# Kernel tuning notes

Measured on AMD Instinct MI355X. Metric: run time of the kernel, lower is better.

Reference implementation:

```python
import jax, jax.numpy as jnp
import numpy as np

B, N, R = 2, 16384, 2048
CA, CS, CP, H = 128, 256, 16, 4
WQ, WK = 32, 128
NW = N // WQ
CH = CA // H
INF = 1e8


def _ln(x, w=None, b=None, eps=1e-5):
    m = jnp.mean(x, axis=-1, keepdims=True)
    v = jnp.var(x, axis=-1, keepdims=True)
    y = (x - m) * jax.lax.rsqrt(v + eps)
    if w is not None:
        y = y * w
    if b is not None:
        y = y + b
    return y


def _gather_res(x, idx):
    # x: [B, R, C], idx: [B, N] -> [B, N, C]  (torch.gather dim=1)
    return jnp.take_along_axis(x, idx[..., None], axis=1)


def _adaln(s, cond, idx, ln_w, Wg, bg, Wb):
    s = _ln(s)                      # LayerNorm, no affine
    cond = _ln(cond, ln_w)          # LayerNorm, weight only
    gate = _gather_res(cond @ Wg + bg, idx)
    bias = _gather_res(cond @ Wb, idx)
    return s * jax.nn.sigmoid(gate) + bias


def setup_inputs():
    key = jax.random.key(0)
    ks = jax.random.split(key, 20)

    def nrm(k, shape, scale=0.02):
        return jax.random.normal(k, shape, jnp.float32) * scale

    # key-window validity mask (keys are wk-wide windows centered on each wq query window)
    centers = np.arange(NW) * WQ + WQ // 2
    kidx = centers[:, None] - WK // 2 + np.arange(WK)[None, :]
    valid = (kidx >= 0) & (kidx < N)                              # [NW, WK]
    atompair_mask = jnp.broadcast_to(jnp.asarray(valid)[None, :, None, :], (B, NW, WQ, WK))

    return dict(
        atom_features=jax.random.normal(ks[0], (B, N, CA), jnp.float32),
        res_features=jax.random.normal(ks[1], (B, R, CS), jnp.float32),
        atompair_features=jax.random.normal(ks[2], (B, NW, WQ, WK, CP), jnp.float32),
        atom_res_idx=jnp.sort(jax.random.randint(ks[3], (B, N), 0, R), axis=1),
        atompos_mask=jnp.ones((B, N), jnp.float32),
        atompair_mask=atompair_mask,
        # attention AdaLN
        a_ln_w=jnp.ones((CS,), jnp.float32),
        a_Wg=nrm(ks[4], (CS, CA)), a_bg=jnp.zeros((CA,), jnp.float32), a_Wb=nrm(ks[5], (CS, CA)),
        # q / kv projections
        q_W=nrm(ks[6], (CA, CA)), q_b=jnp.zeros((CA,), jnp.float32), kv_W=nrm(ks[7], (CA, 2 * CA)),
        # pair bias head: LayerNorm(c_atompair) + Linear(c_atompair -> H, no bias)
        bij_ln_w=jnp.ones((CP,), jnp.float32), bij_ln_b=jnp.zeros((CP,), jnp.float32), bij_W=nrm(ks[8], (CP, H)),
        # residue-conditioned output gate (bias init -2)
        sg_W=nrm(ks[9], (CS, CA)), sg_b=jnp.full((CA,), -2.0, jnp.float32),
        # transition AdaLN + SwiGLU + cond gate
        t_ln_w=jnp.ones((CS,), jnp.float32),
        t_Wg=nrm(ks[10], (CS, CA)), t_bg=jnp.zeros((CA,), jnp.float32), t_Wb=nrm(ks[11], (CS, CA)),
        t_W1=nrm(ks[12], (CA, 2 * CA)), t_W2=nrm(ks[13], (CA, 2 * CA)),
        t_Wc=nrm(ks[14], (CS, CA)), t_bc=jnp.full((CA,), -2.0, jnp.float32),
        t_Wo=nrm(ks[15], (2 * CA, CA)),
    )


def reference(atom_features, res_features, atompair_features, atom_res_idx,
              atompos_mask, atompair_mask,
              a_ln_w, a_Wg, a_bg, a_Wb,
              q_W, q_b, kv_W,
              bij_ln_w, bij_ln_b, bij_W,
              sg_W, sg_b,
              t_ln_w, t_Wg, t_bg, t_Wb,
              t_W1, t_W2, t_Wc, t_bc, t_Wo):
    B_, N_ = atom_features.shape[0], atom_features.shape[1]
    # to_keys index: wk-wide key window centered on each query window (clamped; mask handles edges)
    centers = jnp.arange(NW) * WQ + WQ // 2
    kidx = jnp.clip(centers[:, None] - WK // 2 + jnp.arange(WK)[None, :], 0, N_ - 1)  # [NW, WK]

    # --- attention ---
    s = _adaln(atom_features, res_features, atom_res_idx, a_ln_w, a_Wg, a_bg, a_Wb)
    q = (s @ q_W + q_b).reshape(B_, NW, WQ, H, CH)                 # to_queries + unflatten
    kv = jnp.take(s @ kv_W, kidx, axis=1)                          # to_keys -> [B, NW, WK, 2*CA]
    kv = kv.reshape(B_, NW, WK, 2 * H, CH)
    k, v = kv[..., :H, :], kv[..., H:, :]
    a = jnp.einsum('bnqhc,bnkhc->bnqkh', q, k) / np.sqrt(CH)
    b_ij = _ln(atompair_features, bij_ln_w, bij_ln_b) @ bij_W      # [B, NW, WQ, WK, H]
    a = a + b_ij - INF * (1.0 - atompair_mask.astype(a.dtype)[..., None])
    p = jax.nn.softmax(a, axis=3)                                  # softmax over keys
    attn_out = jnp.einsum('bnqkh,bnkhc->bnqhc', p, v).reshape(B_, N_, CA)
    gate = jax.nn.sigmoid(res_features @ sg_W + sg_b)              # raw res_features (no LN)
    attn_out = attn_out * _gather_res(gate, atom_res_idx)

    atom = atom_features + attn_out * atompos_mask[..., None]

    # --- gather-conditioned transition ---
    t = _adaln(atom, res_features, atom_res_idx, t_ln_w, t_Wg, t_bg, t_Wb)
    b = jax.nn.silu(t @ t_W1) * (t @ t_W2)                          # SwiGLU, n=2
    tg = jax.nn.sigmoid(_gather_res(res_features @ t_Wc + t_bc, atom_res_idx))
    trans = tg * (b @ t_Wo)

    return atom + trans * atompos_mask[..., None]
```

## Files before the change

### kernel.cpp

```cpp
#include <hip/hip_runtime.h>
#include <hip/hip_bf16.h>
#include <string.h>

namespace {

constexpr int Bc  = 2;
constexpr int Nc  = 16384;
constexpr int Rc  = 2048;
constexpr int CAc = 128;
constexpr int CSc = 256;
constexpr int CPc = 16;
constexpr int Hc  = 4;
constexpr int WQc = 32;
constexpr int WKc = 128;
constexpr int NWc = 512;
constexpr float EPSf     = 1e-5f;
constexpr float NEG_INF  = -1e8f;
constexpr float QK_SCALE = 0.17677669529663687f;

constexpr int VT_STRIDE = 16512;
constexpr int VT_BATCH  = 128 * VT_STRIDE;

typedef short bf16x8 __attribute__((ext_vector_type(8)));
typedef float f32x4 __attribute__((ext_vector_type(4)));
typedef unsigned int u32x4 __attribute__((ext_vector_type(4)));

__device__ __forceinline__ float wsum(float v) {
#pragma unroll
  for (int m = 1; m < 64; m <<= 1) v += __shfl_xor(v, m, 64);
  return v;
}
__device__ __forceinline__ float sigm(float x) { return 1.0f / (1.0f + __expf(-x)); }
__device__ __forceinline__ float f4c(const float4& v, int i) {
  return i == 0 ? v.x : i == 1 ? v.y : i == 2 ? v.z : v.w;
}
__device__ __forceinline__ unsigned short bfx(float v) {
  __hip_bfloat16 h = __float2bfloat16(v);
  unsigned short u;
  memcpy(&u, &h, 2);
  return u;
}
__device__ __forceinline__ unsigned pk2(float a, float b) {
  return (unsigned)bfx(a) | ((unsigned)bfx(b) << 16);
}
__device__ __forceinline__ float ubf(unsigned us) {
  unsigned v = us << 16;
  float f;
  memcpy(&f, &v, 4);
  return f;
}
__device__ __forceinline__ bf16x8 ldfrag(const ushort* p) {
  return __builtin_bit_cast(bf16x8, *(const u32x4*)p);
}

__global__ void k_pack_resln(const float* __restrict__ q_W, const float* __restrict__ kv_W,
                             const float* __restrict__ t_W1, const float* __restrict__ t_W2,
                             const float* __restrict__ t_Wo,
                             ushort* __restrict__ qWt, ushort* __restrict__ kvWt,
                             ushort* __restrict__ midWt, ushort* __restrict__ WoT,
                             ushort* __restrict__ vT,
                             const float* __restrict__ res, const float* __restrict__ a_ln_w,
                             const float* __restrict__ t_ln_w, float* __restrict__ lnA,
                             float* __restrict__ lnT) {
  if (blockIdx.x < 704) {
    const int i = blockIdx.x * 256 + threadIdx.x;
    if (i < 16384) {
      const int n = i >> 7, k = i & 127;
      qWt[i] = bfx(q_W[k * 128 + n]);
    } else if (i < 49152) {
      const int i2 = i - 16384;
      const int n = i2 >> 7, k = i2 & 127;
      kvWt[i2] = bfx(kv_W[k * 256 + n]);
    } else if (i < 114688) {
      const int i3 = i - 49152;
      const int n = i3 >> 7, k = i3 & 127;
      midWt[i3] = bfx(n < 256 ? t_W1[k * 256 + n] : t_W2[k * 256 + (n - 256)]);
    } else if (i < 147456) {
      const int i4 = i - 114688;
      const int n = i4 >> 8, k = i4 & 255;
      WoT[i4] = bfx(t_Wo[k * 128 + n]);
    } else if (i < 180224) {
      const int j = i - 147456;
      const int b = j >> 14, rem = j & 16383;
      const int d = rem >> 7, p = rem & 127;
      const int col = (p < 64) ? p : (16384 + p);
      vT[(size_t)b * VT_BATCH + (size_t)d * VT_STRIDE + col] = 0;
    }
  } else {
    const int wid = threadIdx.x >> 6, lane = threadIdx.x & 63;
    const int row = (blockIdx.x - 704) * 4 + wid;
    const float* r = res + (size_t)row * CSc;
    float x[4], s = 0.f, sq = 0.f;
#pragma unroll
    for (int i = 0; i < 4; ++i) { x[i] = r[lane + 64 * i]; s += x[i]; sq += x[i] * x[i]; }
    s = wsum(s); sq = wsum(sq);
    const float mn = s * (1.0f / CSc);
    const float var = sq * (1.0f / CSc) - mn * mn;
    const float rs = rsqrtf(var + EPSf);
#pragma unroll
    for (int i = 0; i < 4; ++i) {
      const int c = lane + 64 * i;
      const float y = (x[i] - mn) * rs;
      lnA[(size_t)row * CSc + c] = y * a_ln_w[c];
      lnT[(size_t)row * CSc + c] = y * t_ln_w[c];
    }
  }
}

__global__ void k_res_gemm(const float* __restrict__ lnA, const float* __restrict__ lnT,
                           const float* __restrict__ res,
                           const float* __restrict__ a_Wg, const float* __restrict__ a_bg,
                           const float* __restrict__ a_Wb,
                           const float* __restrict__ t_Wg, const float* __restrict__ t_bg,
                           const float* __restrict__ t_Wb,
                           const float* __restrict__ sg_W, const float* __restrict__ sg_b,
                           const float* __restrict__ t_Wc, const float* __restrict__ t_bc,
                           float* __restrict__ Ag, float* __restrict__ Ab,
                           float* __restrict__ Tg, float* __restrict__ Tb,
                           float* __restrict__ Sg, float* __restrict__ Tc) {
  __shared__ float tile[32 * CSc];
  const int m = blockIdx.y;
  const float* in = (m < 2) ? lnA : (m < 4) ? lnT : res;
  const float* W  = (m == 0) ? a_Wg : (m == 1) ? a_Wb : (m == 2) ? t_Wg
                  : (m == 3) ? t_Wb : (m == 4) ? sg_W : t_Wc;
  const float* bias = (m == 0) ? a_bg : (m == 2) ? t_bg : (m == 4) ? sg_b
                    : (m == 5) ? t_bc : nullptr;
  const bool sig = (m == 0) || (m == 2) || (m == 4) || (m == 5);
  float* out = (m == 0) ? Ag : (m == 1) ? Ab : (m == 2) ? Tg
             : (m == 3) ? Tb : (m == 4) ? Sg : Tc;
  const int row0 = blockIdx.x * 32;
  const float4* src = (const float4*)(in + (size_t)row0 * CSc);
  float4* dst = (float4*)tile;
#pragma unroll
  for (int k = 0; k < 8; ++k) dst[threadIdx.x + 256 * k] = src[threadIdx.x + 256 * k];
  __syncthreads();
  const int c0 = (threadIdx.x & 31) * 4;
  const int r0 = (threadIdx.x >> 5) * 4;
  float acc[4][4] = {};
  for (int j = 0; j < CSc; j += 4) {
    float4 a[4];
#pragma unroll
    for (int r = 0; r < 4; ++r) a[r] = *(const float4*)&tile[(r0 + r) * CSc + j];
#pragma unroll
    for (int jj = 0; jj < 4; ++jj) {
      const float4 w = *(const float4*)&W[(size_t)(j + jj) * CAc + c0];
#pragma unroll
      for (int r = 0; r < 4; ++r) {
        const float av = f4c(a[r], jj);
        acc[r][0] += av * w.x; acc[r][1] += av * w.y;
        acc[r][2] += av * w.z; acc[r][3] += av * w.w;
      }
    }
  }
  float4 bv = make_float4(0.f, 0.f, 0.f, 0.f);
  if (bias) bv = *(const float4*)&bias[c0];
#pragma unroll
  for (int r = 0; r < 4; ++r) {
    float4 o;
    o.x = acc[r][0] + bv.x; o.y = acc[r][1] + bv.y;
    o.z = acc[r][2] + bv.z; o.w = acc[r][3] + bv.w;
    if (sig) { o.x = sigm(o.x); o.y = sigm(o.y); o.z = sigm(o.z); o.w = sigm(o.w); }
    *(float4*)&out[(size_t)(row0 + r0 + r) * CAc + c0] = o;
  }
}

__global__ void k_adaln16(const float* __restrict__ in, const int* __restrict__ idxG,
                          const float* __restrict__ G, const float* __restrict__ Bb,
                          unsigned* __restrict__ out32) {
  const int wid = threadIdx.x >> 6, lane = threadIdx.x & 63;
  const int row = blockIdx.x * 4 + wid;
  const int b = row >> 14;
  const float* r = in + (size_t)row * CAc;
  const float2 xp = *(const float2*)&r[2 * lane];
  const float s = wsum(xp.x + xp.y);
  const float sq = wsum(xp.x * xp.x + xp.y * xp.y);
  const float mn = s * (1.0f / CAc);
  const float var = sq * (1.0f / CAc) - mn * mn;
  const float rs = rsqrtf(var + EPSf);
  const int base = (b * Rc + idxG[row]) * CAc;
  const float2 g2 = *(const float2*)&G[base + 2 * lane];
  const float2 b2 = *(const float2*)&Bb[base + 2 * lane];
  const float y0 = (xp.x - mn) * rs * g2.x + b2.x;
  const float y1 = (xp.y - mn) * rs * g2.y + b2.y;
  out32[(size_t)row * 64 + lane] = pk2(y0, y1);
}

__global__ __launch_bounds__(256) void k_gemm_qkv(
    const ushort* __restrict__ act16, const ushort* __restrict__ qWt,
    const ushort* __restrict__ kvWt, const float* __restrict__ q_b,
    ushort* __restrict__ q16, ushort* __restrict__ k16, ushort* __restrict__ vT) {
  __shared__ ushort vtile[128][72];
  const int ny = blockIdx.y;
  const int wid = threadIdx.x >> 6, lane = threadIdx.x & 63;
  const int c = lane & 15, s = lane >> 4;
  const int wm = wid & 1, wn = wid >> 1;
  const int base = blockIdx.x * 64;
  const int m0 = base + wm * 32;
  const int nb = wn * 64;
  const ushort* Wt = (ny == 0) ? qWt : kvWt + (ny == 2 ? 128 * 128 : 0);
  f32x4 acc[4][2];
#pragma unroll
  for (int nt = 0; nt < 4; ++nt)
#pragma unroll
    for (int mt = 0; mt < 2; ++mt) { acc[nt][mt][0]=0.f; acc[nt][mt][1]=0.f; acc[nt][mt][2]=0.f; acc[nt][mt][3]=0.f; }
#pragma unroll
  for (int kk = 0; kk < 4; ++kk) {
    const int k0 = kk * 32 + 8 * s;
    bf16x8 bA[2];
#pragma unroll
    for (int mt = 0; mt < 2; ++mt)
      bA[mt] = ldfrag(&act16[(size_t)(m0 + mt * 16 + c) * 128 + k0]);
#pragma unroll
    for (int nt = 0; nt < 4; ++nt) {
      const bf16x8 aW = ldfrag(&Wt[(size_t)(nb + nt * 16 + c) * 128 + k0]);
#pragma unroll
      for (int mt = 0; mt < 2; ++mt)
        acc[nt][mt] = __builtin_amdgcn_mfma_f32_16x16x32_bf16(aW, bA[mt], acc[nt][mt], 0, 0, 0);
    }
  }
#pragma unroll
  for (int nt = 0; nt < 4; ++nt) {
    const int colb = nb + nt * 16 + 4 * s;
    float4 qb4 = make_float4(0.f, 0.f, 0.f, 0.f);
    if (ny == 0) qb4 = *(const float4*)&q_b[colb];
#pragma unroll
    for (int mt = 0; mt < 2; ++mt) {
      const int m = m0 + mt * 16 + c;
      const f32x4 a = acc[nt][mt];
      if (ny == 0) {
        ushort4 u4;
        u4.x = bfx((a[0] + qb4.x) * QK_SCALE); u4.y = bfx((a[1] + qb4.y) * QK_SCALE);
        u4.z = bfx((a[2] + qb4.z) * QK_SCALE); u4.w = bfx((a[3] + qb4.w) * QK_SCALE);
        *(ushort4*)&q16[(size_t)m * 128 + colb] = u4;
      } else if (ny == 1) {
        ushort4 u4;
        u4.x = bfx(a[0]); u4.y = bfx(a[1]); u4.z = bfx(a[2]); u4.w = bfx(a[3]);
        *(ushort4*)&k16[(size_t)m * 128 + colb] = u4;
      } else {
        const int rowl = wm * 32 + mt * 16 + c;
#pragma unroll
        for (int r = 0; r < 4; ++r)
          vtile[colb + r][rowl] = bfx(a[r]);
      }
    }
  }
  if (ny == 2) {
    __syncthreads();
    const int bb2 = base >> 14, nn0 = base & 16383;
    const int t = threadIdx.x;
    const int d = t >> 1, half = t & 1;
    ushort* dst = vT + (size_t)bb2 * VT_BATCH + (size_t)d * VT_STRIDE + 64 + nn0 + half * 32;
    const ushort* srcl = &vtile[d][half * 32];
#pragma unroll
    for (int u = 0; u < 4; ++u)
      *(uint4*)(dst + u * 8) = *(const uint4*)(srcl + u * 8);
  }
}

__global__ __launch_bounds__(256) void k_battn(
    const float* __restrict__ ap, const float* __restrict__ bw,
    const float* __restrict__ bb, const float* __restrict__ bW,
    const ushort* __restrict__ qG, const ushort* __restrict__ kG,
    const ushort* __restrict__ vT,
    const int* __restrict__ idxG, const float* __restrict__ SgG,
    const float* __restrict__ pmask, const float* __restrict__ atomF,
    float* __restrict__ atomO) {
  __shared__ ushort biasL[8192];
  __shared__ float w2s[64], W2sh[4], Cbh[4];
  const int tid = threadIdx.x;
  const int bwid = blockIdx.x >> 1;
  const int half = blockIdx.x & 1;
  const int b = bwid >> 9, w = bwid & 511;
  const size_t bN = (size_t)b * Nc;

  if (tid < 64) w2s[tid] = bw[tid >> 2] * bW[tid];
  __syncthreads();
  if (tid < 4) {
    float a = 0.f, b2 = 0.f;
#pragma unroll
    for (int cp = 0; cp < 16; ++cp) { a += w2s[cp * 4 + tid]; b2 += bb[cp] * bW[cp * 4 + tid]; }
    W2sh[tid] = a; Cbh[tid] = b2;
  }
  __syncthreads();
  const float* apw = ap + (size_t)bwid * (WQc * WKc * CPc) + (size_t)half * (16 * 128 * CPc);
#pragma unroll 2
  for (int u = 0; u < 8; ++u) {
    const int p = tid + 256 * u;
    const int qql = p >> 7, kk = p & 127;
    const float* src = apw + (size_t)p * CPc;
    float sum = 0.f, sq = 0.f, d0 = 0.f, d1 = 0.f, d2 = 0.f, d3 = 0.f;
#pragma unroll
    for (int t = 0; t < 4; ++t) {
      const float4 v4 = *(const float4*)&src[t * 4];
#pragma unroll
      for (int e = 0; e < 4; ++e) {
        const float x = f4c(v4, e);
        const float4 wv = *(const float4*)&w2s[(4 * t + e) * 4];
        sum += x; sq += x * x;
        d0 += x * wv.x; d1 += x * wv.y; d2 += x * wv.z; d3 += x * wv.w;
      }
    }
    const float mn = sum * 0.0625f;
    const float var = sq * 0.0625f - mn * mn;
    const float rs = rsqrtf(var + EPSf);
    const int gk = w * 32 - 48 + kk;
    const float maskt = (gk >= 0 && gk < Nc) ? 0.f : NEG_INF;
    const int mt = kk >> 4, s_ = (kk >> 2) & 3, r_ = kk & 3;
    const int col = s_ * 16 + (qql ^ ((mt & 3) << 2) ^ s_);
    const int base = mt * 256 + col * 4 + r_;
    biasL[base]        = bfx(rs * (d0 - mn * W2sh[0]) + Cbh[0] + maskt);
    biasL[base + 2048] = bfx(rs * (d1 - mn * W2sh[1]) + Cbh[1] + maskt);
    biasL[base + 4096] = bfx(rs * (d2 - mn * W2sh[2]) + Cbh[2] + maskt);
    biasL[base + 6144] = bfx(rs * (d3 - mn * W2sh[3]) + Cbh[3] + maskt);
  }
  __syncthreads();

  const int h = tid >> 6;
  const int lane = tid & 63;
  const int c = lane & 15, s = lane >> 4;

  f32x4 acc[8];
  {
    const ushort* bh = &biasL[h * 2048];
#pragma unroll
    for (int mt = 0; mt < 8; ++mt) {
      const int col = s * 16 + (c ^ ((mt & 3) << 2) ^ s);
      const uint2 pk = *(const uint2*)&bh[mt * 256 + col * 4];
      acc[mt][0] = ubf(pk.x & 0xffff);
      acc[mt][1] = ubf(pk.x >> 16);
      acc[mt][2] = ubf(pk.y & 0xffff);
      acc[mt][3] = ubf(pk.y >> 16);
    }
  }

  const int qq = w * 32 + half * 16 + c;
  const bf16x8 bfragQ = ldfrag(&qG[(bN + qq) * CAc + h * 32 + 8 * s]);
#pragma unroll
  for (int mt = 0; mt < 8; ++mt) {
    int gk = w * 32 - 48 + mt * 16 + c;
    gk = min(max(gk, 0), Nc - 1);
    const bf16x8 afragK = ldfrag(&kG[(bN + gk) * CAc + h * 32 + 8 * s]);
    acc[mt] = __builtin_amdgcn_mfma_f32_16x16x32_bf16(afragK, bfragQ, acc[mt], 0, 0, 0);
  }

  int ppk[8][2];
  {
    float mx = -3e38f;
#pragma unroll
    for (int mt = 0; mt < 8; ++mt)
#pragma unroll
      for (int r = 0; r < 4; ++r) mx = fmaxf(mx, acc[mt][r]);
    mx = fmaxf(mx, __shfl_xor(mx, 16, 64));
    mx = fmaxf(mx, __shfl_xor(mx, 32, 64));
    float sm = 0.f;
#pragma unroll
    for (int mt = 0; mt < 8; ++mt)
#pragma unroll
      for (int r = 0; r < 4; ++r) {
        const float e = __expf(acc[mt][r] - mx);
        acc[mt][r] = e;
        sm += e;
      }
    sm += __shfl_xor(sm, 16, 64);
    sm += __shfl_xor(sm, 32, 64);
    const float inv = 1.0f / sm;
#pragma unroll
    for (int mt = 0; mt < 8; ++mt) {
      ppk[mt][0] = (int)pk2(acc[mt][0] * inv, acc[mt][1] * inv);
      ppk[mt][1] = (int)pk2(acc[mt][2] * inv, acc[mt][3] * inv);
    }
  }

  f32x4 opv[2];
  opv[0][0]=0.f; opv[0][1]=0.f; opv[0][2]=0.f; opv[0][3]=0.f;
  opv[1][0]=0.f; opv[1][1]=0.f; opv[1][2]=0.f; opv[1][3]=0.f;
  const int idxA = 4 * ((((2 * s) & 3) << 4) | c);
  const int idxB = 4 * ((((2 * s + 1) & 3) << 4) | c);
  const ushort* vTb = vT + (size_t)b * VT_BATCH;
#pragma unroll
  for (int ks = 0; ks < 4; ++ks) {
    const int vbase = 64 + w * 32 - 48 + ks * 32 + 8 * s;
    bf16x8 bV[2];
#pragma unroll
    for (int ntd = 0; ntd < 2; ++ntd) {
      const int d = h * 32 + ntd * 16 + c;
      bV[ntd] = ldfrag(&vTb[(size_t)d * VT_STRIDE + vbase]);
    }
    int atv[4];
    {
      const int a0 = __builtin_amdgcn_ds_bpermute(idxA, ppk[2 * ks][0]);
      const int b0 = __builtin_amdgcn_ds_bpermute(idxA, ppk[2 * ks + 1][0]);
      atv[0] = (s < 2) ? a0 : b0;
      const int a1 = __builtin_amdgcn_ds_bpermute(idxA, ppk[2 * ks][1]);
      const int b1 = __builtin_amdgcn_ds_bpermute(idxA, ppk[2 * ks + 1][1]);
      atv[1] = (s < 2) ? a1 : b1;
      const int a2 = __builtin_amdgcn_ds_bpermute(idxB, ppk[2 * ks][0]);
      const int b2 = __builtin_amdgcn_ds_bpermute(idxB, ppk[2 * ks + 1][0]);
      atv[2] = (s < 2) ? a2 : b2;
      const int a3 = __builtin_amdgcn_ds_bpermute(idxB, ppk[2 * ks][1]);
      const int b3 = __builtin_amdgcn_ds_bpermute(idxB, ppk[2 * ks + 1][1]);
      atv[3] = (s < 2) ? a3 : b3;
    }
    const bf16x8 afragP = __builtin_bit_cast(bf16x8, *(const u32x4*)atv);
#pragma unroll
    for (int ntd = 0; ntd < 2; ++ntd)
      opv[ntd] = __builtin_amdgcn_mfma_f32_16x16x32_bf16(afragP, bV[ntd], opv[ntd], 0, 0, 0);
  }

#pragma unroll
  for (int r = 0; r < 4; ++r) {
    const int qr = w * 32 + half * 16 + 4 * s + r;
    const size_t rowg = bN + qr;
    const int residx = idxG[rowg];
    const float pm = pmask[rowg];
    const size_t gbase = ((size_t)b * Rc + residx) * CAc;
#pragma unroll
    for (int ntd = 0; ntd < 2; ++ntd) {
      const int d = h * 32 + ntd * 16 + c;
      const float g = SgG[gbase + d];
      const float af = atomF[rowg * CAc + d];
      atomO[rowg * CAc + d] = af + opv[ntd][r] * g * pm;
    }
  }
}

__global__ __launch_bounds__(256) void k_gemm_mid(
    const ushort* __restrict__ act16, const ushort* __restrict__ midWt,
    ushort* __restrict__ bmid16) {
  const int wid = threadIdx.x >> 6, lane = threadIdx.x & 63;
  const int c = lane & 15, s = lane >> 4;
  const int wm = wid & 1, wn = wid >> 1;
  const int m0 = blockIdx.x * 64 + wm * 32;
  const int nb = blockIdx.y * 64 + wn * 32;
  f32x4 acc1[2][2], acc2[2][2];
#pragma unroll
  for (int nt = 0; nt < 2; ++nt)
#pragma unroll
    for (int mt = 0; mt < 2; ++mt) {
      acc1[nt][mt][0]=0.f; acc1[nt][mt][1]=0.f; acc1[nt][mt][2]=0.f; acc1[nt][mt][3]=0.f;
      acc2[nt][mt][0]=0.f; acc2[nt][mt][1]=0.f; acc2[nt][mt][2]=0.f; acc2[nt][mt][3]=0.f;
    }
#pragma unroll
  for (int kk = 0; kk < 4; ++kk) {
    const int k0 = kk * 32 + 8 * s;
    bf16x8 bA[2];
#pragma unroll
    for (int mt = 0; mt < 2; ++mt)
      bA[mt] = ldfrag(&act16[(size_t)(m0 + mt * 16 + c) * 128 + k0]);
#pragma unroll
    for (int nt = 0; nt < 2; ++nt) {
      const bf16x8 aW1 = ldfrag(&midWt[(size_t)(nb + nt * 16 + c) * 128 + k0]);
      const bf16x8 aW2 = ldfrag(&midWt[(size_t)(256 + nb + nt * 16 + c) * 128 + k0]);
#pragma unroll
      for (int mt = 0; mt < 2; ++mt) {
        acc1[nt][mt] = __builtin_amdgcn_mfma_f32_16x16x32_bf16(aW1, bA[mt], acc1[nt][mt], 0, 0, 0);
        acc2[nt][mt] = __builtin_amdgcn_mfma_f32_16x16x32_bf16(aW2, bA[mt], acc2[nt][mt], 0, 0, 0);
      }
    }
  }
#pragma unroll
  for (int nt = 0; nt < 2; ++nt) {
    const int colb = nb + nt * 16 + 4 * s;
#pragma unroll
    for (int mt = 0; mt < 2; ++mt) {
      const int m = m0 + mt * 16 + c;
      ushort4 u4;
#pragma unroll
      for (int r = 0; r < 4; ++r) {
        const float a1 = acc1[nt][mt][r];
        const float v = a1 * sigm(a1) * acc2[nt][mt][r];
        ((unsigned short*)&u4)[r] = bfx(v);
      }
      *(ushort4*)&bmid16[(size_t)m * 256 + colb] = u4;
    }
  }
}

__global__ __launch_bounds__(256) void k_gemm_out(
    const ushort* __restrict__ bmid16, const ushort* __restrict__ WoT,
    const float* __restrict__ atomw, const int* __restrict__ idxG,
    const float* __restrict__ TcG, const float* __restrict__ pmask,
    float* __restrict__ outG) {
  const int wid = threadIdx.x >> 6, lane = threadIdx.x & 63;
  const int c = lane & 15, s = lane >> 4;
  const int wm = wid & 1, wn = wid >> 1;
  const int m0 = blockIdx.x * 64 + wm * 32;
  const int nb = wn * 64;
  f32x4 acc[4][2];
#pragma unroll
  for (int nt = 0; nt < 4; ++nt)
#pragma unroll
    for (int mt = 0; mt < 2; ++mt) { acc[nt][mt][0]=0.f; acc[nt][mt][1]=0.f; acc[nt][mt][2]=0.f; acc[nt][mt][3]=0.f; }
#pragma unroll
  for (int kk = 0; kk < 8; ++kk) {
    const int k0 = kk * 32 + 8 * s;
    bf16x8 bA[2];
#pragma unroll
    for (int mt = 0; mt < 2; ++mt)
      bA[mt] = ldfrag(&bmid16[(size_t)(m0 + mt * 16 + c) * 256 + k0]);
#pragma unroll
    for (int nt = 0; nt < 4; ++nt) {
      const bf16x8 aW = ldfrag(&WoT[(size_t)(nb + nt * 16 + c) * 256 + k0]);
#pragma unroll
      for (int mt = 0; mt < 2; ++mt)
        acc[nt][mt] = __builtin_amdgcn_mfma_f32_16x16x32_bf16(aW, bA[mt], acc[nt][mt], 0, 0, 0);
    }
  }
#pragma unroll
  for (int mt = 0; mt < 2; ++mt) {
    const int m = m0 + mt * 16 + c;
    const int b = m >> 14;
    const int idx = idxG[m];
    const float pm = pmask[m];
    const size_t tcb = ((size_t)(b * Rc) + idx) * CAc;
#pragma unroll
    for (int nt = 0; nt < 4; ++nt) {
      const int colb = nb + nt * 16 + 4 * s;
      const float4 tc = *(const float4*)&TcG[tcb + colb];
      const float4 at = *(const float4*)&atomw[(size_t)m * CAc + colb];
      float4 o;
      o.x = at.x + tc.x * acc[nt][mt][0] * pm;
      o.y = at.y + tc.y * acc[nt][mt][1] * pm;
      o.z = at.z + tc.z * acc[nt][mt][2] * pm;
      o.w = at.w + tc.w * acc[nt][mt][3] * pm;
      *(float4*)&outG[(size_t)m * CAc + colb] = o;
    }
  }
}

}

extern "C" void kernel_launch(void* const* d_in, const int* in_sizes, int n_in,
                              void* d_out, int out_size, void* d_ws, size_t ws_size,
                              hipStream_t stream) {
  (void)in_sizes; (void)n_in; (void)out_size; (void)ws_size;
  const float* atomF   = (const float*)d_in[0];
  const float* resF    = (const float*)d_in[1];
  const float* apF     = (const float*)d_in[2];
  const int*   idx     = (const int*)d_in[3];
  const float* pmask   = (const float*)d_in[4];
  const float* a_ln_w  = (const float*)d_in[6];
  const float* a_Wg    = (const float*)d_in[7];
  const float* a_bg    = (const float*)d_in[8];
  const float* a_Wb    = (const float*)d_in[9];
  const float* q_W     = (const float*)d_in[10];
  const float* q_b     = (const float*)d_in[11];
  const float* kv_W    = (const float*)d_in[12];
  const float* bij_ln_w= (const float*)d_in[13];
  const float* bij_ln_b= (const float*)d_in[14];
  const float* bij_W   = (const float*)d_in[15];
  const float* sg_W    = (const float*)d_in[16];
  const float* sg_b    = (const float*)d_in[17];
  const float* t_ln_w  = (const float*)d_in[18];
  const float* t_Wg    = (const float*)d_in[19];
  const float* t_bg    = (const float*)d_in[20];
  const float* t_Wb    = (const float*)d_in[21];
  const float* t_W1    = (const float*)d_in[22];
  const float* t_W2    = (const float*)d_in[23];
  const float* t_Wc    = (const float*)d_in[24];
  const float* t_bc    = (const float*)d_in[25];
  const float* t_Wo    = (const float*)d_in[26];

  float* ws = (float*)d_ws;
  float* Ag    = ws;
  float* Ab    = Ag + 524288;
  float* Tg    = Ab + 524288;
  float* Tb    = Tg + 524288;
  float* Sg    = Tb + 524288;
  float* Tc    = Sg + 524288;
  float* lnA   = Tc + 524288;
  float* lnT   = lnA + 1048576;
  ushort* act16  = (ushort*)(lnT + 1048576);
  ushort* q16    = act16 + 4194304;
  ushort* k16    = q16 + 4194304;
  ushort* bmid16 = k16 + 4194304;
  float* atomw   = (float*)(bmid16 + 8388608);
  ushort* qWt    = (ushort*)(atomw + 4194304);
  ushort* kvWt   = qWt + 16384;
  ushort* midWt  = kvWt + 32768;
  ushort* WoT    = midWt + 65536;
  ushort* vT     = WoT + 32768;

  k_pack_resln<<<dim3(1728), dim3(256), 0, stream>>>(
      q_W, kv_W, t_W1, t_W2, t_Wo, qWt, kvWt, midWt, WoT, vT,
      resF, a_ln_w, t_ln_w, lnA, lnT);
  k_res_gemm<<<dim3(Bc * Rc / 32, 6), dim3(256), 0, stream>>>(
      lnA, lnT, resF, a_Wg, a_bg, a_Wb, t_Wg, t_bg, t_Wb, sg_W, sg_b, t_Wc, t_bc,
      Ag, Ab, Tg, Tb, Sg, Tc);
  k_adaln16<<<dim3(Bc * Nc / 4), dim3(256), 0, stream>>>(atomF, idx, Ag, Ab,
                                                         (unsigned*)act16);
  k_gemm_qkv<<<dim3(Bc * Nc / 64, 3), dim3(256), 0, stream>>>(act16, qWt, kvWt, q_b,
                                                              q16, k16, vT);
  k_battn<<<dim3(Bc * NWc * 2), dim3(256), 0, stream>>>(
      apF, bij_ln_w, bij_ln_b, bij_W, q16, k16, vT, idx, Sg, pmask, atomF, atomw);
  k_adaln16<<<dim3(Bc * Nc / 4), dim3(256), 0, stream>>>(atomw, idx, Tg, Tb,
                                                         (unsigned*)act16);
  k_gemm_mid<<<dim3(Bc * Nc / 64, 4), dim3(256), 0, stream>>>(act16, midWt, bmid16);
  k_gemm_out<<<dim3(Bc * Nc / 64), dim3(256), 0, stream>>>(bmid16, WoT, atomw, idx, Tc,
                                                           pmask, (float*)d_out);
}
```

Before: 218.2 us.

## Fuse SwiGLU and output GEMMs via shared memory and store residual in bf16

Merges the transition's SwiGLU mid GEMM and the output projection into one kernel that keeps the 32x256 intermediate in LDS instead of writing it to global memory. The attention-updated atom residual is now stored as bf16, and a new AdaLN variant reads that bf16 input. Together these cut global memory traffic and one launch. The cost is larger per-wave register use in the fused kernel and reduced precision on the residual that feeds the final output.

```diff
diff --git a/kernel.cpp b/kernel.cpp
--- a/kernel.cpp
+++ b/kernel.cpp
@@ -185,6 +185,27 @@
   out32[(size_t)row * 64 + lane] = pk2(y0, y1);
 }
 
+__global__ void k_adaln16b(const unsigned* __restrict__ in32, const int* __restrict__ idxG,
+                           const float* __restrict__ G, const float* __restrict__ Bb,
+                           unsigned* __restrict__ out32) {
+  const int wid = threadIdx.x >> 6, lane = threadIdx.x & 63;
+  const int row = blockIdx.x * 4 + wid;
+  const int b = row >> 14;
+  const unsigned pkx = in32[(size_t)row * 64 + lane];
+  const float x0 = ubf(pkx & 0xffff), x1 = ubf(pkx >> 16);
+  const float s = wsum(x0 + x1);
+  const float sq = wsum(x0 * x0 + x1 * x1);
+  const float mn = s * (1.0f / CAc);
+  const float var = sq * (1.0f / CAc) - mn * mn;
+  const float rs = rsqrtf(var + EPSf);
+  const int base = (b * Rc + idxG[row]) * CAc;
+  const float2 g2 = *(const float2*)&G[base + 2 * lane];
+  const float2 b2 = *(const float2*)&Bb[base + 2 * lane];
+  const float y0 = (x0 - mn) * rs * g2.x + b2.x;
+  const float y1 = (x1 - mn) * rs * g2.y + b2.y;
+  out32[(size_t)row * 64 + lane] = pk2(y0, y1);
+}
+
 __global__ __launch_bounds__(256) void k_gemm_qkv(
     const ushort* __restrict__ act16, const ushort* __restrict__ qWt,
     const ushort* __restrict__ kvWt, const float* __restrict__ q_b,
@@ -264,7 +285,7 @@
     const ushort* __restrict__ vT,
     const int* __restrict__ idxG, const float* __restrict__ SgG,
     const float* __restrict__ pmask, const float* __restrict__ atomF,
-    float* __restrict__ atomO) {
+    ushort* __restrict__ atomO16) {
   __shared__ ushort biasL[8192];
   __shared__ float w2s[64], W2sh[4], Cbh[4];
   const int tid = threadIdx.x;
@@ -419,111 +440,109 @@
       const int d = h * 32 + ntd * 16 + c;
       const float g = SgG[gbase + d];
       const float af = atomF[rowg * CAc + d];
-      atomO[rowg * CAc + d] = af + opv[ntd][r] * g * pm;
-    }
-  }
-}
-
-__global__ __launch_bounds__(256) void k_gemm_mid(
+      atomO16[rowg * CAc + d] = bfx(af + opv[ntd][r] * g * pm);
+    }
+  }
+}
+
+__global__ __launch_bounds__(256) void k_gemm_trans(
     const ushort* __restrict__ act16, const ushort* __restrict__ midWt,
-    ushort* __restrict__ bmid16) {
+    const ushort* __restrict__ WoT, const ushort* __restrict__ atomw16,
+    const int* __restrict__ idxG, const float* __restrict__ TcG,
+    const float* __restrict__ pmask, float* __restrict__ outG) {
+  __shared__ ushort smid[32 * 264];
   const int wid = threadIdx.x >> 6, lane = threadIdx.x & 63;
   const int c = lane & 15, s = lane >> 4;
-  const int wm = wid & 1, wn = wid >> 1;
-  const int m0 = blockIdx.x * 64 + wm * 32;
-  const int nb = blockIdx.y * 64 + wn * 32;
-  f32x4 acc1[2][2], acc2[2][2];
-#pragma unroll
-  for (int nt = 0; nt < 2; ++nt)
-#pragma unroll
-    for (int mt = 0; mt < 2; ++mt) {
-      acc1[nt][mt][0]=0.f; acc1[nt][mt][1]=0.f; acc1[nt][mt][2]=0.f; acc1[nt][mt][3]=0.f;
-      acc2[nt][mt][0]=0.f; acc2[nt][mt][1]=0.f; acc2[nt][mt][2]=0.f; acc2[nt][mt][3]=0.f;
-    }
-#pragma unroll
-  for (int kk = 0; kk < 4; ++kk) {
-    const int k0 = kk * 32 + 8 * s;
-    bf16x8 bA[2];
-#pragma unroll
-    for (int mt = 0; mt < 2; ++mt)
-      bA[mt] = ldfrag(&act16[(size_t)(m0 + mt * 16 + c) * 128 + k0]);
-#pragma unroll
-    for (int nt = 0; nt < 2; ++nt) {
-      const bf16x8 aW1 = ldfrag(&midWt[(size_t)(nb + nt * 16 + c) * 128 + k0]);
-      const bf16x8 aW2 = ldfrag(&midWt[(size_t)(256 + nb + nt * 16 + c) * 128 + k0]);
+  const int m0 = blockIdx.x * 32;
+
+  {
+    const int nb = wid * 64;
+    f32x4 acc1[4][2], acc2[4][2];
+#pragma unroll
+    for (int nt = 0; nt < 4; ++nt)
 #pragma unroll
       for (int mt = 0; mt < 2; ++mt) {
-        acc1[nt][mt] = __builtin_amdgcn_mfma_f32_16x16x32_bf16(aW1, bA[mt], acc1[nt][mt], 0, 0, 0);
-        acc2[nt][mt] = __builtin_amdgcn_mfma_f32_16x16x32_bf16(aW2, bA[mt], acc2[nt][mt], 0, 0, 0);
-      }
-    }
-  }
-#pragma unroll
-  for (int nt = 0; nt < 2; ++nt) {
-    const int colb = nb + nt * 16 + 4 * s;
+        acc1[nt][mt][0]=0.f; acc1[nt][mt][1]=0.f; acc1[nt][mt][2]=0.f; acc1[nt][mt][3]=0.f;
+        acc2[nt][mt][0]=0.f; acc2[nt][mt][1]=0.f; acc2[nt][mt][2]=0.f; acc2[nt][mt][3]=0.f;
+      }
+#pragma unroll
+    for (int kk = 0; kk < 4; ++kk) {
+      const int k0 = kk * 32 + 8 * s;
+      bf16x8 bA[2];
+#pragma unroll
+      for (int mt = 0; mt < 2; ++mt)
+        bA[mt] = ldfrag(&act16[(size_t)(m0 + mt * 16 + c) * 128 + k0]);
+#pragma unroll
+      for (int nt = 0; nt < 4; ++nt) {
+        const bf16x8 aW1 = ldfrag(&midWt[(size_t)(nb + nt * 16 + c) * 128 + k0]);
+        const bf16x8 aW2 = ldfrag(&midWt[(size_t)(256 + nb + nt * 16 + c) * 128 + k0]);
+#pragma unroll
+        for (int mt = 0; mt < 2; ++mt) {
+          acc1[nt][mt] = __builtin_amdgcn_mfma_f32_16x16x32_bf16(aW1, bA[mt], acc1[nt][mt], 0, 0, 0);
+          acc2[nt][mt] = __builtin_amdgcn_mfma_f32_16x16x32_bf16(aW2, bA[mt], acc2[nt][mt], 0, 0, 0);
+        }
+      }
+    }
+#pragma unroll
+    for (int nt = 0; nt < 4; ++nt) {
+      const int colb = nb + nt * 16 + 4 * s;
+#pragma unroll
+      for (int mt = 0; mt < 2; ++mt) {
+        const int ml = mt * 16 + c;
+        ushort4 u4;
+#pragma unroll
+        for (int r = 0; r < 4; ++r) {
+          const float a1 = acc1[nt][mt][r];
+          const float v = a1 * sigm(a1) * acc2[nt][mt][r];
+          ((unsigned short*)&u4)[r] = bfx(v);
+        }
+        *(ushort4*)&smid[ml * 264 + colb] = u4;
+      }
+    }
+  }
+  __syncthreads();
+
+  {
+    const int nbo = wid * 32;
+    f32x4 acc[2][2];
+#pragma unroll
+    for (int nt = 0; nt < 2; ++nt)
+#pragma unroll
+      for (int mt = 0; mt < 2; ++mt) { acc[nt][mt][0]=0.f; acc[nt][mt][1]=0.f; acc[nt][mt][2]=0.f; acc[nt][mt][3]=0.f; }
+#pragma unroll
+    for (int kk = 0; kk < 8; ++kk) {
+      const int k0 = kk * 32 + 8 * s;
+      bf16x8 bA[2];
+#pragma unroll
+      for (int mt = 0; mt < 2; ++mt)
+        bA[mt] = ldfrag(&smid[(mt * 16 + c) * 264 + k0]);
+#pragma unroll
+      for (int nt = 0; nt < 2; ++nt) {
+        const bf16x8 aW = ldfrag(&WoT[(size_t)(nbo + nt * 16 + c) * 256 + k0]);
+#pragma unroll
+        for (int mt = 0; mt < 2; ++mt)
+          acc[nt][mt] = __builtin_amdgcn_mfma_f32_16x16x32_bf16(aW, bA[mt], acc[nt][mt], 0, 0, 0);
+      }
+    }
 #pragma unroll
     for (int mt = 0; mt < 2; ++mt) {
       const int m = m0 + mt * 16 + c;
-      ushort4 u4;
-#pragma unroll
-      for (int r = 0; r < 4; ++r) {
-        const float a1 = acc1[nt][mt][r];
-        const float v = a1 * sigm(a1) * acc2[nt][mt][r];
-        ((unsigned short*)&u4)[r] = bfx(v);
-      }
-      *(ushort4*)&bmid16[(size_t)m * 256 + colb] = u4;
-    }
-  }
-}
-
-__global__ __launch_bounds__(256) void k_gemm_out(
-    const ushort* __restrict__ bmid16, const ushort* __restrict__ WoT,
-    const float* __restrict__ atomw, const int* __restrict__ idxG,
-    const float* __restrict__ TcG, const float* __restrict__ pmask,
-    float* __restrict__ outG) {
-  const int wid = threadIdx.x >> 6, lane = threadIdx.x & 63;
-  const int c = lane & 15, s = lane >> 4;
-  const int wm = wid & 1, wn = wid >> 1;
-  const int m0 = blockIdx.x * 64 + wm * 32;
-  const int nb = wn * 64;
-  f32x4 acc[4][2];
-#pragma unroll
-  for (int nt = 0; nt < 4; ++nt)
-#pragma unroll
-    for (int mt = 0; mt < 2; ++mt) { acc[nt][mt][0]=0.f; acc[nt][mt][1]=0.f; acc[nt][mt][2]=0.f; acc[nt][mt][3]=0.f; }
-#pragma unroll
-  for (int kk = 0; kk < 8; ++kk) {
-    const int k0 = kk * 32 + 8 * s;
-    bf16x8 bA[2];
-#pragma unroll
-    for (int mt = 0; mt < 2; ++mt)
-      bA[mt] = ldfrag(&bmid16[(size_t)(m0 + mt * 16 + c) * 256 + k0]);
-#pragma unroll
-    for (int nt = 0; nt < 4; ++nt) {
-      const bf16x8 aW = ldfrag(&WoT[(size_t)(nb + nt * 16 + c) * 256 + k0]);
-#pragma unroll
-      for (int mt = 0; mt < 2; ++mt)
-        acc[nt][mt] = __builtin_amdgcn_mfma_f32_16x16x32_bf16(aW, bA[mt], acc[nt][mt], 0, 0, 0);
-    }
-  }
-#pragma unroll
-  for (int mt = 0; mt < 2; ++mt) {
-    const int m = m0 + mt * 16 + c;
-    const int b = m >> 14;
-    const int idx = idxG[m];
-    const float pm = pmask[m];
-    const size_t tcb = ((size_t)(b * Rc) + idx) * CAc;
-#pragma unroll
-    for (int nt = 0; nt < 4; ++nt) {
-      const int colb = nb + nt * 16 + 4 * s;
-      const float4 tc = *(const float4*)&TcG[tcb + colb];
-      const float4 at = *(const float4*)&atomw[(size_t)m * CAc + colb];
-      float4 o;
-      o.x = at.x + tc.x * acc[nt][mt][0] * pm;
-      o.y = at.y + tc.y * acc[nt][mt][1] * pm;
-      o.z = at.z + tc.z * acc[nt][mt][2] * pm;
-      o.w = at.w + tc.w * acc[nt][mt][3] * pm;
-      *(float4*)&outG[(size_t)m * CAc + colb] = o;
+      const int b = m >> 14;
+      const int idx = idxG[m];
+      const float pm = pmask[m];
+      const size_t tcb = ((size_t)(b * Rc) + idx) * CAc;
+#pragma unroll
+      for (int nt = 0; nt < 2; ++nt) {
+        const int colb = nbo + nt * 16 + 4 * s;
+        const float4 tc = *(const float4*)&TcG[tcb + colb];
+        const ushort4 at4 = *(const ushort4*)&atomw16[(size_t)m * CAc + colb];
+        float4 o;
+        o.x = ubf(at4.x) + tc.x * acc[nt][mt][0] * pm;
+        o.y = ubf(at4.y) + tc.y * acc[nt][mt][1] * pm;
+        o.z = ubf(at4.z) + tc.z * acc[nt][mt][2] * pm;
+        o.w = ubf(at4.w) + tc.w * acc[nt][mt][3] * pm;
+        *(float4*)&outG[(size_t)m * CAc + colb] = o;
+      }
     }
   }
 }
@@ -573,9 +592,8 @@
   ushort* act16  = (ushort*)(lnT + 1048576);
   ushort* q16    = act16 + 4194304;
   ushort* k16    = q16 + 4194304;
-  ushort* bmid16 = k16 + 4194304;
-  float* atomw   = (float*)(bmid16 + 8388608);
-  ushort* qWt    = (ushort*)(atomw + 4194304);
+  ushort* atomw16= k16 + 4194304;
+  ushort* qWt    = atomw16 + 4194304;
   ushort* kvWt   = qWt + 16384;
   ushort* midWt  = kvWt + 32768;
   ushort* WoT    = midWt + 65536;
@@ -592,10 +610,9 @@
   k_gemm_qkv<<<dim3(Bc * Nc / 64, 3), dim3(256), 0, stream>>>(act16, qWt, kvWt, q_b,
                                                               q16, k16, vT);
   k_battn<<<dim3(Bc * NWc * 2), dim3(256), 0, stream>>>(
-      apF, bij_ln_w, bij_ln_b, bij_W, q16, k16, vT, idx, Sg, pmask, atomF, atomw);
-  k_adaln16<<<dim3(Bc * Nc / 4), dim3(256), 0, stream>>>(atomw, idx, Tg, Tb,
-                                                         (unsigned*)act16);
-  k_gemm_mid<<<dim3(Bc * Nc / 64, 4), dim3(256), 0, stream>>>(act16, midWt, bmid16);
-  k_gemm_out<<<dim3(Bc * Nc / 64), dim3(256), 0, stream>>>(bmid16, WoT, atomw, idx, Tc,
-                                                           pmask, (float*)d_out);
-}
+      apF, bij_ln_w, bij_ln_b, bij_W, q16, k16, vT, idx, Sg, pmask, atomF, atomw16);
+  k_adaln16b<<<dim3(Bc * Nc / 4), dim3(256), 0, stream>>>((unsigned*)atomw16, idx, Tg, Tb,
+                                                          (unsigned*)act16);
+  k_gemm_trans<<<dim3(Bc * Nc / 32), dim3(256), 0, stream>>>(
+      act16, midWt, WoT, atomw16, idx, Tc, pmask, (float*)d_out);
+}
```

After: 206.7 us. 5.3% less time.
